# Optimization experiments

Measured on AMD Instinct MI355X. Metric: run time of the kernel, lower is better.

The kernel has to match this reference:

```python
import jax, jax.numpy as jnp
import numpy as np

# Quantization constants from the original module
X_ZP = -66   # int8 zero point
Y_ZP = 160   # uint8 zero point


def setup_inputs() -> dict:
    key = jax.random.key(0)
    k1, k2 = jax.random.split(key)
    # x: [7, B, M, K] int8 in [-128, 127]
    x = jax.random.randint(k1, (7, 8, 512, 1024), -128, 128, dtype=jnp.int32).astype(jnp.int8)
    # y: [B, K, N] uint8 in [0, 255]
    y = jax.random.randint(k2, (8, 1024, 512), 0, 256, dtype=jnp.int32).astype(jnp.uint8)
    return {
        "x": x,
        "y": y,
        "x_scale": jnp.float32(0.03),
        "y_scale": jnp.float32(0.025),
    }


def reference(x, y, x_scale, y_scale):
    # dequantize_per_tensor: (q - zero_point) * scale
    xf = (x.astype(jnp.float32) - jnp.float32(X_ZP)) * x_scale   # [7, B, M, K]
    yf = (y.astype(jnp.float32) - jnp.float32(Y_ZP)) * y_scale   # [B, K, N]
    # torch.matmul broadcast: [7,B,M,K] @ [B,K,N] -> [7,B,M,N]
    return jnp.einsum('gbmk,bkn->gbmn', xf, yf)
```

## Files before the change

kernel.cpp:

```cpp
#include <hip/hip_runtime.h>
#include <stdint.h>

#define AS1 __attribute__((address_space(1)))
#define AS3 __attribute__((address_space(3)))

typedef int v4i __attribute__((ext_vector_type(4)));

constexpr int G = 7, B = 8, M = 512, N = 512, K = 1024;
constexpr int GBn = G * B;

constexpr size_t YT_BYTES = (size_t)B * N * K;
constexpr size_t CS_CNT   = (size_t)B * N;
constexpr size_t WS_NEEDED = YT_BYTES + CS_CNT * 4;

__global__ __launch_bounds__(256) void transpose_pack_y(const int* __restrict__ y,
                                                        signed char* __restrict__ yt) {
    __shared__ unsigned char tile[64][80];
    int n0 = blockIdx.x * 64;
    int k0 = blockIdx.y * 64;
    int b  = blockIdx.z;
    int t  = threadIdx.x;

    int r  = t >> 2;
    int c0 = (t & 3) * 16;
    const int* src = y + ((size_t)b * K + k0 + r) * N + n0 + c0;
    uint32_t p[4];
#pragma unroll
    for (int q = 0; q < 4; ++q) {
        int4 v = ((const int4*)src)[q];
        p[q] =  (uint32_t)((v.x & 255) ^ 128)
             | ((uint32_t)((v.y & 255) ^ 128) << 8)
             | ((uint32_t)((v.z & 255) ^ 128) << 16)
             | ((uint32_t)((v.w & 255) ^ 128) << 24);
    }
    *(uint4*)&tile[r][c0] = make_uint4(p[0], p[1], p[2], p[3]);
    __syncthreads();

    int nl = t >> 2;
    int kc = (t & 3) * 16;
    uint32_t q[4];
#pragma unroll
    for (int w = 0; w < 4; ++w) {
        uint32_t b0 = tile[kc + w * 4 + 0][nl];
        uint32_t b1 = tile[kc + w * 4 + 1][nl];
        uint32_t b2 = tile[kc + w * 4 + 2][nl];
        uint32_t b3 = tile[kc + w * 4 + 3][nl];
        q[w] = b0 | (b1 << 8) | (b2 << 16) | (b3 << 24);
    }
    *(uint4*)(yt + ((size_t)b * N + n0 + nl) * K + k0 + kc) = make_uint4(q[0], q[1], q[2], q[3]);
}

__global__ __launch_bounds__(256) void colsum_y(const signed char* __restrict__ yt,
                                                int* __restrict__ colsum) {
    int wave = threadIdx.x >> 6, lane = threadIdx.x & 63;
    int rr = blockIdx.x * 4 + wave;
    uint4 u = *(const uint4*)(yt + (size_t)rr * K + lane * 16);
    uint32_t wds[4] = {u.x, u.y, u.z, u.w};
    int s = 0;
#pragma unroll
    for (int q = 0; q < 4; ++q) {
        uint32_t w = wds[q];
        s += (int)(signed char)(w) + (int)(signed char)(w >> 8)
           + (int)(signed char)(w >> 16) + (int)(signed char)(w >> 24);
    }
#pragma unroll
    for (int off = 32; off > 0; off >>= 1) s += __shfl_down(s, off, 64);
    if (lane == 0) colsum[rr] = s;
}

__global__ __launch_bounds__(512, 4) void gemm_i8(const int* __restrict__ x,
                                                  const signed char* __restrict__ yt,
                                                  const int* __restrict__ colsum,
                                                  const float* __restrict__ xsp,
                                                  const float* __restrict__ ysp,
                                                  float* __restrict__ out) {
    __shared__ signed char As[2][128 * 64];
    __shared__ signed char Bs[2][256 * 64];
    __shared__ int rsm[128];

    int mt = blockIdx.x;
    int nt = blockIdx.y;
    int gb = blockIdx.z;
    int b  = gb & 7;
    int tid = threadIdx.x, wave = tid >> 6, lane = tid & 63;
    int wm = (wave >> 2) * 64, wn = (wave & 3) * 64;

    int arow = tid >> 2;
    const int* xr = x + ((size_t)(gb * M + mt * 128 + arow)) * K + (tid & 3) * 16;
    int aslot = (tid & 3) ^ ((arow >> 1) & 3);
    int aoff  = arow * 64 + aslot * 16;

    int bslot = (lane & 3) ^ ((lane >> 3) & 3);
    const signed char* Bb = yt + ((size_t)(b * N + nt * 256 + wave * 16 + (lane >> 2))) * K + bslot * 16;

    int fr = lane & 15, q = lane >> 4;
    int fko = (q ^ ((fr >> 1) & 3)) * 16;

    v4i acc[4][4];
#pragma unroll
    for (int i = 0; i < 4; ++i)
#pragma unroll
        for (int j = 0; j < 4; ++j) acc[i][j] = (v4i){0, 0, 0, 0};

    int rs_part = 0;

    int4 xv[4];
#pragma unroll
    for (int h = 0; h < 4; ++h) xv[h] = ((const int4*)xr)[h];
#pragma unroll
    for (int c = 0; c < 2; ++c)
        __builtin_amdgcn_global_load_lds((const AS1 uint32_t*)(Bb + (size_t)c * 128 * K),
                                         (AS3 uint32_t*)(&Bs[0][0] + c * 8192 + wave * 1024), 16, 0, 0);
    {
        uint32_t pw[4];
#pragma unroll
        for (int h = 0; h < 4; ++h) {
            int4 v = xv[h];
            rs_part += v.x + v.y + v.z + v.w;
            pw[h] =  (uint32_t)(v.x & 255) | ((uint32_t)(v.y & 255) << 8)
                  | ((uint32_t)(v.z & 255) << 16) | ((uint32_t)(v.w & 255) << 24);
        }
        *(uint4*)(&As[0][0] + aoff) = make_uint4(pw[0], pw[1], pw[2], pw[3]);
    }

    for (int s = 0; s < 16; ++s) {
        int cur = s & 1;
        __syncthreads();

        int4 xn[4];
        if (s < 15) {
            const int* xs_ = xr + (s + 1) * 64;
#pragma unroll
            for (int h = 0; h < 4; ++h) xn[h] = ((const int4*)xs_)[h];
#pragma unroll
            for (int c = 0; c < 2; ++c)
                __builtin_amdgcn_global_load_lds((const AS1 uint32_t*)(Bb + (size_t)c * 128 * K + (s + 1) * 64),
                                                 (AS3 uint32_t*)(&Bs[cur ^ 1][0] + c * 8192 + wave * 1024), 16, 0, 0);
        }

        v4i af[4], bf[4];
#pragma unroll
        for (int i = 0; i < 4; ++i)
            af[i] = *(const v4i*)(&As[cur][0] + (wm + i * 16 + fr) * 64 + fko);
#pragma unroll
        for (int j = 0; j < 4; ++j)
            bf[j] = *(const v4i*)(&Bs[cur][0] + (wn + j * 16 + fr) * 64 + fko);
#pragma unroll
        for (int i = 0; i < 4; ++i)
#pragma unroll
            for (int j = 0; j < 4; ++j)
                acc[i][j] = __builtin_amdgcn_mfma_i32_16x16x64_i8(af[i], bf[j], acc[i][j], 0, 0, 0);

        if (s < 15) {
            uint32_t pw[4];
#pragma unroll
            for (int h = 0; h < 4; ++h) {
                int4 v = xn[h];
                rs_part += v.x + v.y + v.z + v.w;
                pw[h] =  (uint32_t)(v.x & 255) | ((uint32_t)(v.y & 255) << 8)
                      | ((uint32_t)(v.z & 255) << 16) | ((uint32_t)(v.w & 255) << 24);
            }
            *(uint4*)(&As[cur ^ 1][0] + aoff) = make_uint4(pw[0], pw[1], pw[2], pw[3]);
        }
    }

    rs_part += __shfl_down(rs_part, 1, 64);
    rs_part += __shfl_down(rs_part, 2, 64);
    if ((lane & 3) == 0) rsm[arow] = rs_part;
    __syncthreads();

    float sc = xsp[0] * ysp[0];
    int colL = lane & 15;
    int rowQ = (lane >> 4) * 4;
    float* outg = out + (size_t)gb * M * N;
    const int* cs = colsum + b * N;
#pragma unroll
    for (int i = 0; i < 4; ++i) {
#pragma unroll
        for (int r = 0; r < 4; ++r) {
            int row_l = wm + i * 16 + rowQ + r;
            int row_g = mt * 128 + row_l;
            int rsv = rsm[row_l];
#pragma unroll
            for (int j = 0; j < 4; ++j) {
                int col_g = nt * 256 + wn + j * 16 + colL;
                int t = acc[i][j][r] - 32 * rsv + 66 * cs[col_g] - 2162688;
                outg[(size_t)row_g * N + col_g] = sc * (float)t;
            }
        }
    }
}

__global__ __launch_bounds__(256) void naive_kernel(const int* __restrict__ x,
                                                    const int* __restrict__ y,
                                                    const float* __restrict__ xsp,
                                                    const float* __restrict__ ysp,
                                                    float* __restrict__ out) {
    size_t idx = (size_t)blockIdx.x * 256 + threadIdx.x;
    int n  = (int)(idx & 511);
    int m  = (int)((idx >> 9) & 511);
    int gb = (int)(idx >> 18);
    int b  = gb & 7;
    const int* xr = x + ((size_t)gb * M + m) * K;
    const int* yc = y + (size_t)b * K * N + n;
    int dot = 0, sx = 0, sy = 0;
    for (int k = 0; k < K; ++k) {
        int a = xr[k];
        int c = yc[(size_t)k * N];
        dot += a * c; sx += a; sy += c;
    }
    float s = xsp[0] * ysp[0];
    out[idx] = s * (float)(dot - 160 * sx + 66 * sy - 10813440);
}

extern "C" void kernel_launch(void* const* d_in, const int* in_sizes, int n_in,
                              void* d_out, int out_size, void* d_ws, size_t ws_size,
                              hipStream_t stream) {
    const int*   x  = (const int*)d_in[0];
    const int*   y  = (const int*)d_in[1];
    const float* xs = (const float*)d_in[2];
    const float* ys = (const float*)d_in[3];
    float* out = (float*)d_out;

    if (ws_size < WS_NEEDED) {
        naive_kernel<<<(14680064 + 255) / 256, 256, 0, stream>>>(x, y, xs, ys, out);
        return;
    }

    char* ws = (char*)d_ws;
    signed char* yt = (signed char*)ws;
    int* colsum = (int*)(ws + YT_BYTES);

    transpose_pack_y<<<dim3(N / 64, K / 64, B), 256, 0, stream>>>(y, yt);
    colsum_y<<<(B * N) / 4, 256, 0, stream>>>(yt, colsum);
    gemm_i8<<<dim3(M / 128, N / 256, GBn), 512, 0, stream>>>(x, yt, colsum, xs, ys, out);
}
```

Baseline: 228.3 us.

## Keep full-K A tile in LDS and stream Y fragments directly from global

The GEMM is restructured so each block loads and packs a 64-row by full-K slice of x into LDS once, computes the row sums up front, and then covers all 512 output columns. Each wave streams its B fragments straight from global or L2 instead of staging them in double-buffered LDS, which removes the per-step barriers. The separate colsum kernel is folded into the transpose kernel through atomics, with a small zeroing kernel added in front. In exchange, x is read by far fewer blocks, but every wave now performs uncoalesced-ish global B loads on the MFMA critical path with no prefetch, and the 64KB LDS tile may limit occupancy.

```diff
diff --git a/kernel.cpp b/kernel.cpp
--- a/kernel.cpp
+++ b/kernel.cpp
@@ -13,8 +13,13 @@
 constexpr size_t CS_CNT   = (size_t)B * N;
 constexpr size_t WS_NEEDED = YT_BYTES + CS_CNT * 4;
 
+__global__ __launch_bounds__(256) void zero_colsum(int* __restrict__ cs) {
+    cs[blockIdx.x * 256 + threadIdx.x] = 0;
+}
+
 __global__ __launch_bounds__(256) void transpose_pack_y(const int* __restrict__ y,
-                                                        signed char* __restrict__ yt) {
+                                                        signed char* __restrict__ yt,
+                                                        int* __restrict__ colsum) {
     __shared__ unsigned char tile[64][80];
     int n0 = blockIdx.x * 64;
     int k0 = blockIdx.y * 64;
@@ -48,144 +53,102 @@
         q[w] = b0 | (b1 << 8) | (b2 << 16) | (b3 << 24);
     }
     *(uint4*)(yt + ((size_t)b * N + n0 + nl) * K + k0 + kc) = make_uint4(q[0], q[1], q[2], q[3]);
-}
-
-__global__ __launch_bounds__(256) void colsum_y(const signed char* __restrict__ yt,
-                                                int* __restrict__ colsum) {
-    int wave = threadIdx.x >> 6, lane = threadIdx.x & 63;
-    int rr = blockIdx.x * 4 + wave;
-    uint4 u = *(const uint4*)(yt + (size_t)rr * K + lane * 16);
-    uint32_t wds[4] = {u.x, u.y, u.z, u.w};
+
     int s = 0;
 #pragma unroll
-    for (int q = 0; q < 4; ++q) {
-        uint32_t w = wds[q];
-        s += (int)(signed char)(w) + (int)(signed char)(w >> 8)
-           + (int)(signed char)(w >> 16) + (int)(signed char)(w >> 24);
-    }
-#pragma unroll
-    for (int off = 32; off > 0; off >>= 1) s += __shfl_down(s, off, 64);
-    if (lane == 0) colsum[rr] = s;
-}
-
-__global__ __launch_bounds__(512, 4) void gemm_i8(const int* __restrict__ x,
-                                                  const signed char* __restrict__ yt,
-                                                  const int* __restrict__ colsum,
-                                                  const float* __restrict__ xsp,
-                                                  const float* __restrict__ ysp,
-                                                  float* __restrict__ out) {
-    __shared__ signed char As[2][128 * 64];
-    __shared__ signed char Bs[2][256 * 64];
-    __shared__ int rsm[128];
+    for (int w = 0; w < 4; ++w) {
+        uint32_t v = q[w];
+        s += (int)(signed char)(v) + (int)(signed char)(v >> 8)
+           + (int)(signed char)(v >> 16) + (int)(signed char)(v >> 24);
+    }
+    s += __shfl_down(s, 1, 64);
+    s += __shfl_down(s, 2, 64);
+    if ((t & 3) == 0) atomicAdd(&colsum[b * N + n0 + nl], s);
+}
+
+__global__ __launch_bounds__(512, 4) void gemm_fused(const int* __restrict__ x,
+                                                     const signed char* __restrict__ yt,
+                                                     const int* __restrict__ colsum,
+                                                     const float* __restrict__ xsp,
+                                                     const float* __restrict__ ysp,
+                                                     float* __restrict__ out) {
+    __shared__ signed char A[64 * 1024];
+    __shared__ int rsm[64];
 
     int mt = blockIdx.x;
-    int nt = blockIdx.y;
-    int gb = blockIdx.z;
+    int gb = blockIdx.y;
     int b  = gb & 7;
-    int tid = threadIdx.x, wave = tid >> 6, lane = tid & 63;
-    int wm = (wave >> 2) * 64, wn = (wave & 3) * 64;
-
-    int arow = tid >> 2;
-    const int* xr = x + ((size_t)(gb * M + mt * 128 + arow)) * K + (tid & 3) * 16;
-    int aslot = (tid & 3) ^ ((arow >> 1) & 3);
-    int aoff  = arow * 64 + aslot * 16;
-
-    int bslot = (lane & 3) ^ ((lane >> 3) & 3);
-    const signed char* Bb = yt + ((size_t)(b * N + nt * 256 + wave * 16 + (lane >> 2))) * K + bslot * 16;
-
-    int fr = lane & 15, q = lane >> 4;
-    int fko = (q ^ ((fr >> 1) & 3)) * 16;
-
-    v4i acc[4][4];
-#pragma unroll
-    for (int i = 0; i < 4; ++i)
-#pragma unroll
-        for (int j = 0; j < 4; ++j) acc[i][j] = (v4i){0, 0, 0, 0};
-
-    int rs_part = 0;
-
-    int4 xv[4];
-#pragma unroll
-    for (int h = 0; h < 4; ++h) xv[h] = ((const int4*)xr)[h];
-#pragma unroll
-    for (int c = 0; c < 2; ++c)
-        __builtin_amdgcn_global_load_lds((const AS1 uint32_t*)(Bb + (size_t)c * 128 * K),
-                                         (AS3 uint32_t*)(&Bs[0][0] + c * 8192 + wave * 1024), 16, 0, 0);
+    int t  = threadIdx.x;
+
     {
-        uint32_t pw[4];
-#pragma unroll
-        for (int h = 0; h < 4; ++h) {
-            int4 v = xv[h];
-            rs_part += v.x + v.y + v.z + v.w;
-            pw[h] =  (uint32_t)(v.x & 255) | ((uint32_t)(v.y & 255) << 8)
-                  | ((uint32_t)(v.z & 255) << 16) | ((uint32_t)(v.w & 255) << 24);
-        }
-        *(uint4*)(&As[0][0] + aoff) = make_uint4(pw[0], pw[1], pw[2], pw[3]);
-    }
-
-    for (int s = 0; s < 16; ++s) {
-        int cur = s & 1;
-        __syncthreads();
-
-        int4 xn[4];
-        if (s < 15) {
-            const int* xs_ = xr + (s + 1) * 64;
-#pragma unroll
-            for (int h = 0; h < 4; ++h) xn[h] = ((const int4*)xs_)[h];
-#pragma unroll
-            for (int c = 0; c < 2; ++c)
-                __builtin_amdgcn_global_load_lds((const AS1 uint32_t*)(Bb + (size_t)c * 128 * K + (s + 1) * 64),
-                                                 (AS3 uint32_t*)(&Bs[cur ^ 1][0] + c * 8192 + wave * 1024), 16, 0, 0);
-        }
-
-        v4i af[4], bf[4];
-#pragma unroll
-        for (int i = 0; i < 4; ++i)
-            af[i] = *(const v4i*)(&As[cur][0] + (wm + i * 16 + fr) * 64 + fko);
-#pragma unroll
-        for (int j = 0; j < 4; ++j)
-            bf[j] = *(const v4i*)(&Bs[cur][0] + (wn + j * 16 + fr) * 64 + fko);
-#pragma unroll
-        for (int i = 0; i < 4; ++i)
-#pragma unroll
-            for (int j = 0; j < 4; ++j)
-                acc[i][j] = __builtin_amdgcn_mfma_i32_16x16x64_i8(af[i], bf[j], acc[i][j], 0, 0, 0);
-
-        if (s < 15) {
+        int r = t >> 3;
+        int c = t & 7;
+        const int* xr = x + ((size_t)(gb * M + mt * 64 + r)) * K + c * 128;
+        int rs = 0;
+#pragma unroll
+        for (int j = 0; j < 8; ++j) {
             uint32_t pw[4];
 #pragma unroll
             for (int h = 0; h < 4; ++h) {
-                int4 v = xn[h];
-                rs_part += v.x + v.y + v.z + v.w;
+                int4 v = ((const int4*)(xr + j * 16))[h];
+                rs += v.x + v.y + v.z + v.w;
                 pw[h] =  (uint32_t)(v.x & 255) | ((uint32_t)(v.y & 255) << 8)
                       | ((uint32_t)(v.z & 255) << 16) | ((uint32_t)(v.w & 255) << 24);
             }
-            *(uint4*)(&As[cur ^ 1][0] + aoff) = make_uint4(pw[0], pw[1], pw[2], pw[3]);
+            int phys = (c * 8 + j) ^ (r & 7);
+            *(uint4*)(A + r * 1024 + phys * 16) = make_uint4(pw[0], pw[1], pw[2], pw[3]);
         }
-    }
-
-    rs_part += __shfl_down(rs_part, 1, 64);
-    rs_part += __shfl_down(rs_part, 2, 64);
-    if ((lane & 3) == 0) rsm[arow] = rs_part;
+        rs += __shfl_down(rs, 1, 64);
+        rs += __shfl_down(rs, 2, 64);
+        rs += __shfl_down(rs, 4, 64);
+        if (c == 0) rsm[r] = rs;
+    }
     __syncthreads();
 
+    int w = t >> 6, lane = t & 63;
+    int wn = w * 64;
+    int fr = lane & 15, q = lane >> 4;
+
+    const signed char* Bb = yt + ((size_t)(b * N + wn + fr)) * K + q * 16;
+
+    v4i acc[4][4];
+#pragma unroll
+    for (int i = 0; i < 4; ++i)
+#pragma unroll
+        for (int j = 0; j < 4; ++j) acc[i][j] = (v4i){0, 0, 0, 0};
+
+#pragma unroll
+    for (int s = 0; s < 16; ++s) {
+        v4i bf[4], af[4];
+#pragma unroll
+        for (int j = 0; j < 4; ++j)
+            bf[j] = *(const v4i*)(Bb + (size_t)j * 16 * K + s * 64);
+#pragma unroll
+        for (int i = 0; i < 4; ++i)
+            af[i] = *(const v4i*)(A + (i * 16 + fr) * 1024 + ((s * 4 + q) ^ (fr & 7)) * 16);
+#pragma unroll
+        for (int i = 0; i < 4; ++i)
+#pragma unroll
+            for (int j = 0; j < 4; ++j)
+                acc[i][j] = __builtin_amdgcn_mfma_i32_16x16x64_i8(af[i], bf[j], acc[i][j], 0, 0, 0);
+    }
+
     float sc = xsp[0] * ysp[0];
-    int colL = lane & 15;
-    int rowQ = (lane >> 4) * 4;
+    int colL = fr;
+    int rowQ = q * 4;
     float* outg = out + (size_t)gb * M * N;
     const int* cs = colsum + b * N;
 #pragma unroll
     for (int i = 0; i < 4; ++i) {
 #pragma unroll
         for (int r = 0; r < 4; ++r) {
-            int row_l = wm + i * 16 + rowQ + r;
-            int row_g = mt * 128 + row_l;
-            int rsv = rsm[row_l];
+            int row_g = mt * 64 + i * 16 + rowQ + r;
+            int rsv = rsm[i * 16 + rowQ + r];
 #pragma unroll
             for (int j = 0; j < 4; ++j) {
-                int col_g = nt * 256 + wn + j * 16 + colL;
-                int t = acc[i][j][r] - 32 * rsv + 66 * cs[col_g] - 2162688;
-                outg[(size_t)row_g * N + col_g] = sc * (float)t;
+                int col_g = wn + j * 16 + colL;
+                int v = acc[i][j][r] - 32 * rsv + 66 * cs[col_g] - 2162688;
+                outg[(size_t)row_g * N + col_g] = sc * (float)v;
             }
         }
     }
@@ -231,7 +194,7 @@
     signed char* yt = (signed char*)ws;
     int* colsum = (int*)(ws + YT_BYTES);
 
-    transpose_pack_y<<<dim3(N / 64, K / 64, B), 256, 0, stream>>>(y, yt);
-    colsum_y<<<(B * N) / 4, 256, 0, stream>>>(yt, colsum);
-    gemm_i8<<<dim3(M / 128, N / 256, GBn), 512, 0, stream>>>(x, yt, colsum, xs, ys, out);
-}
+    zero_colsum<<<CS_CNT / 256, 256, 0, stream>>>(colsum);
+    transpose_pack_y<<<dim3(N / 64, K / 64, B), 256, 0, stream>>>(y, yt, colsum);
+    gemm_fused<<<dim3(M / 64, GBn), 512, 0, stream>>>(x, yt, colsum, xs, ys, out);
+}
```

New measurement: 234.3 us. +2.6%, slower.
